# Performance work log

Hardware: AMD Instinct MI355X
Metric: run time of the kernel (lower is better)

## Reference

```python
import jax, jax.numpy as jnp
import numpy as np
import math

B, S, DM, DQ, DK, DV = 4, 4096, 512, 512, 512, 512
MASKED = True


def setup_inputs() -> dict:
    key = jax.random.key(0)
    ks = jax.random.split(key, 9)
    s = 1.0 / math.sqrt(DM)  # ~ torch Linear init scale
    return {
        "q_in": jax.random.normal(ks[0], (B, S, DM), jnp.float32),
        "k_in": jax.random.normal(ks[1], (B, S, DM), jnp.float32),
        "v_in": jax.random.normal(ks[2], (B, S, DM), jnp.float32),
        "Wq": jax.random.uniform(ks[3], (DQ, DM), jnp.float32, -s, s),
        "bq": jax.random.uniform(ks[4], (DQ,), jnp.float32, -s, s),
        "Wk": jax.random.uniform(ks[5], (DK, DM), jnp.float32, -s, s),
        "bk": jax.random.uniform(ks[6], (DK,), jnp.float32, -s, s),
        "Wv": jax.random.uniform(ks[7], (DV, DM), jnp.float32, -s, s),
        "bv": jax.random.uniform(ks[8], (DV,), jnp.float32, -s, s),
    }


def reference(q_in, k_in, v_in, Wq, bq, Wk, bk, Wv, bv):
    # Linear projections (torch Linear: x @ W.T + b)
    q = jnp.einsum("bsm,qm->bsq", q_in, Wq) + bq  # [B,S,DQ]
    k = jnp.einsum("bsm,km->bsk", k_in, Wk) + bk  # [B,S,DK]
    v = jnp.einsum("bsm,vm->bsv", v_in, Wv) + bv  # [B,S,DV]

    scale = 1.0 / math.sqrt(k.shape[-1])
    scores = jnp.einsum("bqd,bkd->bqk", q, k) * scale  # [B,S,S]
    if MASKED:
        # Faithful to torch.tril on the scores: upper triangle set to 0 (NOT -inf)
        tri = jnp.tril(jnp.ones((scores.shape[1], scores.shape[2]), bool))
        scores = jnp.where(tri, scores, jnp.zeros((), scores.dtype))
    attn = jax.nn.softmax(scores, axis=-1)
    return jnp.einsum("bqk,bkv->bqv", attn, v)  # [B,S,DV]
```

## Files before the change

kernel.cpp:

```cpp
#include <hip/hip_runtime.h>

typedef unsigned short u16;
typedef unsigned int   u32;
typedef __bf16  bf16x8 __attribute__((ext_vector_type(8)));
typedef u16     u16x8  __attribute__((ext_vector_type(8)));
typedef float   f32x4  __attribute__((ext_vector_type(4)));

#define S_LEN   4096
#define DMODEL  512
#define NBATCH  4
#define NTILE   32
#define NPAIR   528
#define SCALE   0.044194173824159216f

__device__ __forceinline__ u16 f2bf(float x){
  u32 u = __float_as_uint(x);
  return (u16)((u + 0x7fffu + ((u >> 16) & 1u)) >> 16);
}
__device__ __forceinline__ float bf2f(u16 u){ return __uint_as_float(((u32)u) << 16); }

__device__ __forceinline__ void gload_lds16(const void* g, void* l){
  __builtin_amdgcn_global_load_lds((const __attribute__((address_space(1))) void*)g,
                                   (__attribute__((address_space(3))) void*)l, 16, 0, 0);
}

__global__ __launch_bounds__(256) void cast3_kernel(const float* __restrict__ a,
                                                    const float* __restrict__ b,
                                                    const float* __restrict__ c,
                                                    u16* oa, u16* ob, u16* oc, int n8){
  int z = blockIdx.y;
  const float* in = (z == 0) ? a : (z == 1) ? b : c;
  u16* out = (z == 0) ? oa : (z == 1) ? ob : oc;
  int i = blockIdx.x * 256 + threadIdx.x;
  int stride = gridDim.x * 256;
  for (; i < n8; i += stride){
    const float4* p = (const float4*)in + (size_t)i * 2;
    float4 x = p[0], y = p[1];
    ushort4 o0 = make_ushort4(f2bf(x.x), f2bf(x.y), f2bf(x.z), f2bf(x.w));
    ushort4 o1 = make_ushort4(f2bf(y.x), f2bf(y.y), f2bf(y.z), f2bf(y.w));
    ((ushort4*)out)[(size_t)i*2]   = o0;
    ((ushort4*)out)[(size_t)i*2+1] = o1;
  }
}

__global__ __launch_bounds__(256) void zero_kernel(float* __restrict__ p, int n){
  int i = blockIdx.x * 256 + threadIdx.x;
  if (i < n) p[i] = 0.f;
}

__global__ __launch_bounds__(256) void proj_kernel(
    const u16* __restrict__ qx, const u16* __restrict__ kx, const u16* __restrict__ vx,
    const u16* __restrict__ Wq, const u16* __restrict__ Wk, const u16* __restrict__ Wv,
    const float* __restrict__ bq, const float* __restrict__ bk, const float* __restrict__ bv,
    u16* Qb, u16* Kb, u16* Vb)
{
  __shared__ __align__(16) u16 ldsA[4096], ldsB[4096];
  int z = blockIdx.z;
  const u16* X = (z==0) ? qx : (z==1) ? kx : vx;
  const u16* W = (z==0) ? Wq : (z==1) ? Wk : Wv;
  const float* bias = (z==0) ? bq : (z==1) ? bk : bv;
  u16* Y = (z==0) ? Qb : (z==1) ? Kb : Vb;

  int cn = blockIdx.x, rm = blockIdx.y;
  int t = threadIdx.x, w = t >> 6, l = t & 63, wr = w >> 1, wc = w & 1;
  f32x4 acc[4][4];
  #pragma unroll
  for (int m = 0; m < 4; m++)
    #pragma unroll
    for (int n = 0; n < 4; n++) acc[m][n] = (f32x4){0.f,0.f,0.f,0.f};

  const u16* A = X + (size_t)rm * 128 * DMODEL;
  const u16* B = W + (size_t)cn * 128 * DMODEL;
  int srow = l >> 2, scol = (l & 3) * 8;
  int lo = l & 15, hi = l >> 4;
  for (int s = 0; s < 16; s++){
    #pragma unroll
    for (int cc = 0; cc < 2; ++cc){
      int c = w + cc * 4;
      gload_lds16(A + (size_t)(c*16 + srow)*DMODEL + s*32 + scol, ldsA + c*512);
      gload_lds16(B + (size_t)(c*16 + srow)*DMODEL + s*32 + scol, ldsB + c*512);
    }
    __syncthreads();
    bf16x8 fa[4], fb[4];
    #pragma unroll
    for (int m = 0; m < 4; m++) fa[m] = *(const bf16x8*)(ldsA + (wr*64 + m*16 + lo)*32 + hi*8);
    #pragma unroll
    for (int n = 0; n < 4; n++) fb[n] = *(const bf16x8*)(ldsB + (wc*64 + n*16 + lo)*32 + hi*8);
    #pragma unroll
    for (int m = 0; m < 4; m++)
      #pragma unroll
      for (int n = 0; n < 4; n++)
        acc[m][n] = __builtin_amdgcn_mfma_f32_16x16x32_bf16(fa[m], fb[n], acc[m][n], 0, 0, 0);
    __syncthreads();
  }

  #pragma unroll
  for (int n = 0; n < 4; n++){
    int col = cn*128 + wc*64 + n*16 + lo;
    float bs = bias[col];
    #pragma unroll
    for (int m = 0; m < 4; m++){
      int row0 = rm*128 + wr*64 + m*16 + hi*4;
      #pragma unroll
      for (int j = 0; j < 4; j++)
        Y[(size_t)(row0 + j) * DMODEL + col] = f2bf(acc[m][n][j] + bs);
    }
  }
}

__global__ __launch_bounds__(256) void transpose_kernel(const u16* __restrict__ V,
                                                        u16* __restrict__ Vt)
{
  __shared__ u16 tile[64][66];
  int k0 = blockIdx.x * 64, c0 = blockIdx.y * 64, b = blockIdx.z;
  int t = threadIdx.x;
  #pragma unroll
  for (int i = 0; i < 16; i++){
    int idx = i*256 + t; int r = idx >> 6, c = idx & 63;
    tile[r][c] = V[((size_t)b*S_LEN + k0 + r) * DMODEL + c0 + c];
  }
  __syncthreads();
  #pragma unroll
  for (int i = 0; i < 16; i++){
    int idx = i*256 + t; int r = idx >> 6, c = idx & 63;
    Vt[((size_t)b*DMODEL + c0 + r) * S_LEN + k0 + c] = tile[c][r];
  }
}

__global__ __launch_bounds__(256) void vpart_kernel(const u16* __restrict__ V,
                                                    float* __restrict__ part){
  int t = blockIdx.x, b = blockIdx.y, c = threadIdx.x;
  const u16* base = V + ((size_t)b*S_LEN + t*128) * DMODEL;
  float s0 = 0.f, s1 = 0.f;
  for (int k = 0; k < 128; k++){
    s0 += bf2f(base[(size_t)k*DMODEL + c]);
    s1 += bf2f(base[(size_t)k*DMODEL + 256 + c]);
  }
  part[((size_t)b*NTILE + t)*DMODEL + c]       = s0;
  part[((size_t)b*NTILE + t)*DMODEL + 256 + c] = s1;
}

__global__ void suffix_kernel(const float* __restrict__ part, float* __restrict__ sufx){
  int b = blockIdx.x, c = threadIdx.x;
  float s = 0.f;
  for (int t = NTILE - 1; t >= 0; t--){
    sufx[((size_t)b*NTILE + t)*DMODEL + c] = s;
    s += part[((size_t)b*NTILE + t)*DMODEL + c];
  }
}

__global__ __launch_bounds__(64) void score_kernel(const u16* __restrict__ Q,
                                                   const u16* __restrict__ K,
                                                   u16* __restrict__ P,
                                                   float* __restrict__ Z)
{
  __shared__ __align__(16) u16 ldsA[2][2048], ldsB[2][2048];
  int flat = blockIdx.x;
  int w = (flat & 7) * 1056 + (flat >> 3);
  int b = w / 2112, r = w % 2112;
  int tp = (int)((sqrtf(1.f + 2.f*(float)r) - 1.f) * 0.5f);
  while (2*(tp+1)*(tp+2) <= r) tp++;
  while (2*tp*(tp+1) > r) tp--;
  int rem = r - 2*tp*(tp+1);
  int qi, ki;
  if (rem < 2*tp + 2){ qi = 2*tp; ki = rem; } else { qi = 2*tp + 1; ki = rem - (2*tp + 2); }

  int l = threadIdx.x;
  int lr = l >> 2, lc = (l & 3) * 8;
  int lo = l & 15, hi = l >> 4;

  const u16* A = Q + ((size_t)b*S_LEN + (size_t)qi*64) * DMODEL;
  const u16* B = K + ((size_t)b*S_LEN + (size_t)ki*64) * DMODEL;

  f32x4 acc[4][4];
  #pragma unroll
  for (int m = 0; m < 4; m++)
    #pragma unroll
    for (int n = 0; n < 4; n++) acc[m][n] = (f32x4){0.f,0.f,0.f,0.f};

#define SC_STAGE(tt, buf) { \
    int s32 = (tt)*32; \
    _Pragma("unroll") \
    for (int c = 0; c < 4; c++){ \
      gload_lds16(A + (size_t)(c*16 + lr)*DMODEL + s32 + lc, &ldsA[buf][c*512]); \
      gload_lds16(B + (size_t)(c*16 + lr)*DMODEL + s32 + lc, &ldsB[buf][c*512]); \
    } }

  if (ki <= qi){
    SC_STAGE(0, 0);
    #pragma unroll 2
    for (int tt = 0; tt < 16; ++tt){
      int cur = tt & 1;
      asm volatile("s_waitcnt lgkmcnt(0)" ::: "memory");
      if (tt < 15){
        SC_STAGE(tt + 1, cur ^ 1);
        asm volatile("s_waitcnt vmcnt(8)" ::: "memory");
      } else {
        asm volatile("s_waitcnt vmcnt(0)" ::: "memory");
      }
      __builtin_amdgcn_sched_barrier(0);
      bf16x8 fa[4], fb[4];
      #pragma unroll
      for (int m = 0; m < 4; m++) fa[m] = *(const bf16x8*)(&ldsA[cur][(m*16 + lo)*32 + hi*8]);
      #pragma unroll
      for (int n = 0; n < 4; n++) fb[n] = *(const bf16x8*)(&ldsB[cur][(n*16 + lo)*32 + hi*8]);
      #pragma unroll
      for (int m = 0; m < 4; m++)
        #pragma unroll
        for (int n = 0; n < 4; n++)
          acc[m][n] = __builtin_amdgcn_mfma_f32_16x16x32_bf16(fa[m], fb[n], acc[m][n], 0, 0, 0);
    }
  }
#undef SC_STAGE

  int qt = qi >> 1, kt = ki >> 1;
  u16* Pt = P + ((size_t)b*NPAIR + (size_t)qt*(qt+1)/2 + kt) * 16384
              + (size_t)(qi & 1) * 64 * 128 + (size_t)(ki & 1) * 64;
  #pragma unroll
  for (int m = 0; m < 4; m++){
    #pragma unroll
    for (int j = 0; j < 4; j++){
      int row = m*16 + hi*4 + j;
      int grow = qi*64 + row;
      float rsum = 0.f;
      #pragma unroll
      for (int n = 0; n < 4; n++){
        int col = n*16 + lo;
        int gcol = ki*64 + col;
        float s = (gcol > grow) ? 0.f : acc[m][n][j] * SCALE;
        u16 pb = f2bf(__expf(s));
        Pt[(size_t)row*128 + col] = pb;
        rsum += bf2f(pb);
      }
      rsum += __shfl_xor(rsum, 1);
      rsum += __shfl_xor(rsum, 2);
      rsum += __shfl_xor(rsum, 4);
      rsum += __shfl_xor(rsum, 8);
      if (lo == 0) atomicAdd(&Z[(size_t)b*S_LEN + grow], rsum);
    }
  }
}

__global__ __launch_bounds__(64) void pv_kernel(const u16* __restrict__ P,
                                                const u16* __restrict__ Vt,
                                                const float* __restrict__ sufx,
                                                const float* __restrict__ Z,
                                                float* __restrict__ out)
{
  __shared__ __align__(16) u16 ldsA[2][2048], ldsB[2][2048];
  int flat = (blockIdx.z*64 + blockIdx.y)*8 + blockIdx.x;
  int w = (flat & 7) * 256 + (flat >> 3);
  int b  = w >> 9;
  int qip = (w >> 3) & 63;
  int qi  = (qip & 1) ? (qip >> 1) : 63 - (qip >> 1);
  int ci  = w & 7;
  int qt  = qi >> 1;

  int l = threadIdx.x;
  int lr = l >> 2, lc = (l & 3) * 8;
  int lo = l & 15, hi = l >> 4;

  const u16* Abase = P + ((size_t)b*NPAIR + (size_t)qt*(qt+1)/2) * 16384
                       + (size_t)(qi & 1) * 64 * 128;
  const u16* Bbase = Vt + ((size_t)b*DMODEL + (size_t)ci*64) * S_LEN;

  f32x4 acc[4][4];
  #pragma unroll
  for (int m = 0; m < 4; m++)
    #pragma unroll
    for (int n = 0; n < 4; n++) acc[m][n] = (f32x4){0.f,0.f,0.f,0.f};

  int nstep = (qt + 1) * 4;

#define PV_STAGE(tt, buf) { \
    int kt_ = (tt) >> 2, s_ = ((tt) & 3) * 32; \
    const u16* A_ = Abase + (size_t)kt_*16384 + s_; \
    const u16* B_ = Bbase + kt_*128 + s_; \
    _Pragma("unroll") \
    for (int c = 0; c < 4; c++){ \
      gload_lds16(A_ + (size_t)(c*16 + lr)*128 + lc, &ldsA[buf][c*512]); \
      gload_lds16(B_ + (size_t)(c*16 + lr)*S_LEN + lc, &ldsB[buf][c*512]); \
    } }

  PV_STAGE(0, 0);
  #pragma unroll 2
  for (int tt = 0; tt < nstep; ++tt){
    int cur = tt & 1;
    asm volatile("s_waitcnt lgkmcnt(0)" ::: "memory");
    if (tt + 1 < nstep){
      PV_STAGE(tt + 1, cur ^ 1);
      asm volatile("s_waitcnt vmcnt(8)" ::: "memory");
    } else {
      asm volatile("s_waitcnt vmcnt(0)" ::: "memory");
    }
    __builtin_amdgcn_sched_barrier(0);
    bf16x8 fa[4], fb[4];
    #pragma unroll
    for (int m = 0; m < 4; m++) fa[m] = *(const bf16x8*)(&ldsA[cur][(m*16 + lo)*32 + hi*8]);
    #pragma unroll
    for (int n = 0; n < 4; n++) fb[n] = *(const bf16x8*)(&ldsB[cur][(n*16 + lo)*32 + hi*8]);
    #pragma unroll
    for (int m = 0; m < 4; m++)
      #pragma unroll
      for (int n = 0; n < 4; n++)
        acc[m][n] = __builtin_amdgcn_mfma_f32_16x16x32_bf16(fa[m], fb[n], acc[m][n], 0, 0, 0);
  }
#undef PV_STAGE

  float zadd = (float)(S_LEN - (qt + 1) * 128);
  const float* suf = sufx + ((size_t)b*NTILE + qt)*DMODEL + ci*64;
  const float* Zp  = Z + (size_t)b*S_LEN + (size_t)qi*64;
  float* O = out + ((size_t)b*S_LEN + (size_t)qi*64) * DMODEL + ci*64;
  #pragma unroll
  for (int m = 0; m < 4; m++){
    #pragma unroll
    for (int j = 0; j < 4; j++){
      int row = m*16 + hi*4 + j;
      float rz = 1.f / (Zp[row] + zadd);
      #pragma unroll
      for (int n = 0; n < 4; n++){
        int col = n*16 + lo;
        O[(size_t)row*DMODEL + col] = (acc[m][n][j] + suf[col]) * rz;
      }
    }
  }
}

extern "C" void kernel_launch(void* const* d_in, const int* in_sizes, int n_in,
                              void* d_out, int out_size, void* d_ws, size_t ws_size,
                              hipStream_t stream)
{
  const float* q_in = (const float*)d_in[0];
  const float* k_in = (const float*)d_in[1];
  const float* v_in = (const float*)d_in[2];
  const float* Wq   = (const float*)d_in[3];
  const float* bq   = (const float*)d_in[4];
  const float* Wk   = (const float*)d_in[5];
  const float* bk   = (const float*)d_in[6];
  const float* Wv   = (const float*)d_in[7];
  const float* bv   = (const float*)d_in[8];
  float* out = (float*)d_out;
  char*  ws  = (char*)d_ws;

  const size_t NTOK  = (size_t)NBATCH * S_LEN;
  const size_t TEN_B = NTOK * DMODEL * 2;

  size_t off = 0;
  u16* Wq_b = (u16*)(ws + off); off += DMODEL*DMODEL*2;
  u16* Wk_b = (u16*)(ws + off); off += DMODEL*DMODEL*2;
  u16* Wv_b = (u16*)(ws + off); off += DMODEL*DMODEL*2;
  size_t uoff = off;
  u16* qx = (u16*)(ws + uoff);
  u16* kx = qx + NTOK*DMODEL;
  u16* vx = kx + NTOK*DMODEL;
  u16* Pbuf = (u16*)(ws + uoff);
  size_t usize = (size_t)NBATCH * NPAIR * 16384 * 2;
  off = uoff + usize;
  u16* Qb  = (u16*)(ws + off); off += TEN_B;
  u16* Kb  = (u16*)(ws + off); off += TEN_B;
  u16* Vb  = (u16*)(ws + off); off += TEN_B;
  u16* Vtb = (u16*)(ws + off); off += TEN_B;
  float* part = (float*)(ws + off); off += (size_t)NBATCH*NTILE*DMODEL*4;
  float* sufx = (float*)(ws + off); off += (size_t)NBATCH*NTILE*DMODEL*4;
  float* Zful = (float*)(ws + off); off += (size_t)NBATCH*S_LEN*4;

  int n8_big = (int)(NTOK * DMODEL / 8);
  int n8_w   = DMODEL * DMODEL / 8;
  cast3_kernel<<<dim3(2048, 3), 256, 0, stream>>>(q_in, k_in, v_in, qx, kx, vx, n8_big);
  cast3_kernel<<<dim3(128, 3), 256, 0, stream>>>(Wq, Wk, Wv, Wq_b, Wk_b, Wv_b, n8_w);
  zero_kernel<<<(NBATCH*S_LEN + 255)/256, 256, 0, stream>>>(Zful, NBATCH*S_LEN);

  proj_kernel<<<dim3(DMODEL/128, (unsigned)(NTOK/128), 3), 256, 0, stream>>>(
      qx, kx, vx, Wq_b, Wk_b, Wv_b, bq, bk, bv, Qb, Kb, Vb);

  transpose_kernel<<<dim3(S_LEN/64, DMODEL/64, NBATCH), 256, 0, stream>>>(Vb, Vtb);
  vpart_kernel<<<dim3(NTILE, NBATCH), 256, 0, stream>>>(Vb, part);
  suffix_kernel<<<NBATCH, DMODEL, 0, stream>>>(part, sufx);

  score_kernel<<<8448, 64, 0, stream>>>(Qb, Kb, Pbuf, Zful);
  pv_kernel<<<dim3(8, 64, NBATCH), 64, 0, stream>>>(Pbuf, Vtb, sufx, Zful, out);
}
```

Before: 399.2 us.

## Load MFMA fragments directly from global memory instead of staging through LDS

The projection, score and PV GEMM kernels stop staging tiles through LDS with global_load_lds. Each lane now loads its bf16x8 MFMA operand fragments straight from global memory into registers, using a two-set register double buffer. The projection kernel also shrinks from 256-thread 128x128 tiles to 64-thread 64x64 tiles. This removes LDS traffic, waitcnt handling and barriers, at the cost of strided, less coalesced global loads, lost intra-block reuse, and higher register pressure.

```diff
diff --git a/kernel.cpp b/kernel.cpp
--- a/kernel.cpp
+++ b/kernel.cpp
@@ -19,10 +19,15 @@
 }
 __device__ __forceinline__ float bf2f(u16 u){ return __uint_as_float(((u32)u) << 16); }
 
-__device__ __forceinline__ void gload_lds16(const void* g, void* l){
-  __builtin_amdgcn_global_load_lds((const __attribute__((address_space(1))) void*)g,
-                                   (__attribute__((address_space(3))) void*)l, 16, 0, 0);
-}
+#define MFMA16(aa, bb) { _Pragma("unroll") \
+  for (int m_ = 0; m_ < 4; m_++){ _Pragma("unroll") \
+    for (int n_ = 0; n_ < 4; n_++) \
+      acc[m_][n_] = __builtin_amdgcn_mfma_f32_16x16x32_bf16(aa[m_], bb[n_], acc[m_][n_], 0, 0, 0); } }
+
+#define LOADQK(s_, aa, bb) { _Pragma("unroll") \
+  for (int m_ = 0; m_ < 4; m_++){ \
+    aa[m_] = *(const bf16x8*)(Ap + (size_t)m_*16*DMODEL + (s_)*32); \
+    bb[m_] = *(const bf16x8*)(Bp + (size_t)m_*16*DMODEL + (s_)*32); } }
 
 __global__ __launch_bounds__(256) void cast3_kernel(const float* __restrict__ a,
                                                     const float* __restrict__ b,
@@ -48,13 +53,12 @@
   if (i < n) p[i] = 0.f;
 }
 
-__global__ __launch_bounds__(256) void proj_kernel(
+__global__ __launch_bounds__(64) void proj_kernel(
     const u16* __restrict__ qx, const u16* __restrict__ kx, const u16* __restrict__ vx,
     const u16* __restrict__ Wq, const u16* __restrict__ Wk, const u16* __restrict__ Wv,
     const float* __restrict__ bq, const float* __restrict__ bk, const float* __restrict__ bv,
     u16* Qb, u16* Kb, u16* Vb)
 {
-  __shared__ __align__(16) u16 ldsA[4096], ldsB[4096];
   int z = blockIdx.z;
   const u16* X = (z==0) ? qx : (z==1) ? kx : vx;
   const u16* W = (z==0) ? Wq : (z==1) ? Wk : Wv;
@@ -62,45 +66,33 @@
   u16* Y = (z==0) ? Qb : (z==1) ? Kb : Vb;
 
   int cn = blockIdx.x, rm = blockIdx.y;
-  int t = threadIdx.x, w = t >> 6, l = t & 63, wr = w >> 1, wc = w & 1;
+  int l = threadIdx.x, lo = l & 15, hi = l >> 4;
+
   f32x4 acc[4][4];
   #pragma unroll
   for (int m = 0; m < 4; m++)
     #pragma unroll
     for (int n = 0; n < 4; n++) acc[m][n] = (f32x4){0.f,0.f,0.f,0.f};
 
-  const u16* A = X + (size_t)rm * 128 * DMODEL;
-  const u16* B = W + (size_t)cn * 128 * DMODEL;
-  int srow = l >> 2, scol = (l & 3) * 8;
-  int lo = l & 15, hi = l >> 4;
-  for (int s = 0; s < 16; s++){
-    #pragma unroll
-    for (int cc = 0; cc < 2; ++cc){
-      int c = w + cc * 4;
-      gload_lds16(A + (size_t)(c*16 + srow)*DMODEL + s*32 + scol, ldsA + c*512);
-      gload_lds16(B + (size_t)(c*16 + srow)*DMODEL + s*32 + scol, ldsB + c*512);
-    }
-    __syncthreads();
-    bf16x8 fa[4], fb[4];
-    #pragma unroll
-    for (int m = 0; m < 4; m++) fa[m] = *(const bf16x8*)(ldsA + (wr*64 + m*16 + lo)*32 + hi*8);
-    #pragma unroll
-    for (int n = 0; n < 4; n++) fb[n] = *(const bf16x8*)(ldsB + (wc*64 + n*16 + lo)*32 + hi*8);
-    #pragma unroll
-    for (int m = 0; m < 4; m++)
-      #pragma unroll
-      for (int n = 0; n < 4; n++)
-        acc[m][n] = __builtin_amdgcn_mfma_f32_16x16x32_bf16(fa[m], fb[n], acc[m][n], 0, 0, 0);
-    __syncthreads();
+  const u16* Ap = X + ((size_t)rm*64 + lo) * DMODEL + hi*8;
+  const u16* Bp = W + ((size_t)cn*64 + lo) * DMODEL + hi*8;
+  bf16x8 a0[4], b0[4], a1[4], b1[4];
+  LOADQK(0, a0, b0);
+  #pragma unroll
+  for (int t2 = 0; t2 < 16; t2 += 2){
+    LOADQK(t2+1, a1, b1);
+    MFMA16(a0, b0);
+    if (t2 + 2 < 16) LOADQK(t2+2, a0, b0);
+    MFMA16(a1, b1);
   }
 
   #pragma unroll
   for (int n = 0; n < 4; n++){
-    int col = cn*128 + wc*64 + n*16 + lo;
+    int col = cn*64 + n*16 + lo;
     float bs = bias[col];
     #pragma unroll
     for (int m = 0; m < 4; m++){
-      int row0 = rm*128 + wr*64 + m*16 + hi*4;
+      int row0 = rm*64 + m*16 + hi*4;
       #pragma unroll
       for (int j = 0; j < 4; j++)
         Y[(size_t)(row0 + j) * DMODEL + col] = f2bf(acc[m][n][j] + bs);
@@ -154,7 +146,6 @@
                                                    u16* __restrict__ P,
                                                    float* __restrict__ Z)
 {
-  __shared__ __align__(16) u16 ldsA[2][2048], ldsB[2][2048];
   int flat = blockIdx.x;
   int w = (flat & 7) * 1056 + (flat >> 3);
   int b = w / 2112, r = w % 2112;
@@ -165,12 +156,7 @@
   int qi, ki;
   if (rem < 2*tp + 2){ qi = 2*tp; ki = rem; } else { qi = 2*tp + 1; ki = rem - (2*tp + 2); }
 
-  int l = threadIdx.x;
-  int lr = l >> 2, lc = (l & 3) * 8;
-  int lo = l & 15, hi = l >> 4;
-
-  const u16* A = Q + ((size_t)b*S_LEN + (size_t)qi*64) * DMODEL;
-  const u16* B = K + ((size_t)b*S_LEN + (size_t)ki*64) * DMODEL;
+  int l = threadIdx.x, lo = l & 15, hi = l >> 4;
 
   f32x4 acc[4][4];
   #pragma unroll
@@ -178,40 +164,19 @@
     #pragma unroll
     for (int n = 0; n < 4; n++) acc[m][n] = (f32x4){0.f,0.f,0.f,0.f};
 
-#define SC_STAGE(tt, buf) { \
-    int s32 = (tt)*32; \
-    _Pragma("unroll") \
-    for (int c = 0; c < 4; c++){ \
-      gload_lds16(A + (size_t)(c*16 + lr)*DMODEL + s32 + lc, &ldsA[buf][c*512]); \
-      gload_lds16(B + (size_t)(c*16 + lr)*DMODEL + s32 + lc, &ldsB[buf][c*512]); \
-    } }
-
   if (ki <= qi){
-    SC_STAGE(0, 0);
-    #pragma unroll 2
-    for (int tt = 0; tt < 16; ++tt){
-      int cur = tt & 1;
-      asm volatile("s_waitcnt lgkmcnt(0)" ::: "memory");
-      if (tt < 15){
-        SC_STAGE(tt + 1, cur ^ 1);
-        asm volatile("s_waitcnt vmcnt(8)" ::: "memory");
-      } else {
-        asm volatile("s_waitcnt vmcnt(0)" ::: "memory");
-      }
-      __builtin_amdgcn_sched_barrier(0);
-      bf16x8 fa[4], fb[4];
-      #pragma unroll
-      for (int m = 0; m < 4; m++) fa[m] = *(const bf16x8*)(&ldsA[cur][(m*16 + lo)*32 + hi*8]);
-      #pragma unroll
-      for (int n = 0; n < 4; n++) fb[n] = *(const bf16x8*)(&ldsB[cur][(n*16 + lo)*32 + hi*8]);
-      #pragma unroll
-      for (int m = 0; m < 4; m++)
-        #pragma unroll
-        for (int n = 0; n < 4; n++)
-          acc[m][n] = __builtin_amdgcn_mfma_f32_16x16x32_bf16(fa[m], fb[n], acc[m][n], 0, 0, 0);
+    const u16* Ap = Q + ((size_t)b*S_LEN + (size_t)qi*64 + lo) * DMODEL + hi*8;
+    const u16* Bp = K + ((size_t)b*S_LEN + (size_t)ki*64 + lo) * DMODEL + hi*8;
+    bf16x8 a0[4], b0[4], a1[4], b1[4];
+    LOADQK(0, a0, b0);
+    #pragma unroll
+    for (int t2 = 0; t2 < 16; t2 += 2){
+      LOADQK(t2+1, a1, b1);
+      MFMA16(a0, b0);
+      if (t2 + 2 < 16) LOADQK(t2+2, a0, b0);
+      MFMA16(a1, b1);
     }
   }
-#undef SC_STAGE
 
   int qt = qi >> 1, kt = ki >> 1;
   u16* Pt = P + ((size_t)b*NPAIR + (size_t)qt*(qt+1)/2 + kt) * 16384
@@ -247,7 +212,6 @@
                                                 const float* __restrict__ Z,
                                                 float* __restrict__ out)
 {
-  __shared__ __align__(16) u16 ldsA[2][2048], ldsB[2][2048];
   int flat = (blockIdx.z*64 + blockIdx.y)*8 + blockIdx.x;
   int w = (flat & 7) * 256 + (flat >> 3);
   int b  = w >> 9;
@@ -256,13 +220,11 @@
   int ci  = w & 7;
   int qt  = qi >> 1;
 
-  int l = threadIdx.x;
-  int lr = l >> 2, lc = (l & 3) * 8;
-  int lo = l & 15, hi = l >> 4;
-
-  const u16* Abase = P + ((size_t)b*NPAIR + (size_t)qt*(qt+1)/2) * 16384
-                       + (size_t)(qi & 1) * 64 * 128;
-  const u16* Bbase = Vt + ((size_t)b*DMODEL + (size_t)ci*64) * S_LEN;
+  int l = threadIdx.x, lo = l & 15, hi = l >> 4;
+
+  const u16* Ap = P + ((size_t)b*NPAIR + (size_t)qt*(qt+1)/2) * 16384
+                    + (size_t)(qi & 1) * 64 * 128 + (size_t)lo * 128 + hi*8;
+  const u16* Bp = Vt + ((size_t)b*DMODEL + (size_t)ci*64 + lo) * S_LEN + hi*8;
 
   f32x4 acc[4][4];
   #pragma unroll
@@ -272,40 +234,22 @@
 
   int nstep = (qt + 1) * 4;
 
-#define PV_STAGE(tt, buf) { \
-    int kt_ = (tt) >> 2, s_ = ((tt) & 3) * 32; \
-    const u16* A_ = Abase + (size_t)kt_*16384 + s_; \
-    const u16* B_ = Bbase + kt_*128 + s_; \
+#define LOADPV(tt_, aa, bb) { int kt_ = (tt_) >> 2, s4_ = ((tt_) & 3) * 32; \
     _Pragma("unroll") \
-    for (int c = 0; c < 4; c++){ \
-      gload_lds16(A_ + (size_t)(c*16 + lr)*128 + lc, &ldsA[buf][c*512]); \
-      gload_lds16(B_ + (size_t)(c*16 + lr)*S_LEN + lc, &ldsB[buf][c*512]); \
-    } }
-
-  PV_STAGE(0, 0);
-  #pragma unroll 2
-  for (int tt = 0; tt < nstep; ++tt){
-    int cur = tt & 1;
-    asm volatile("s_waitcnt lgkmcnt(0)" ::: "memory");
-    if (tt + 1 < nstep){
-      PV_STAGE(tt + 1, cur ^ 1);
-      asm volatile("s_waitcnt vmcnt(8)" ::: "memory");
-    } else {
-      asm volatile("s_waitcnt vmcnt(0)" ::: "memory");
-    }
-    __builtin_amdgcn_sched_barrier(0);
-    bf16x8 fa[4], fb[4];
-    #pragma unroll
-    for (int m = 0; m < 4; m++) fa[m] = *(const bf16x8*)(&ldsA[cur][(m*16 + lo)*32 + hi*8]);
-    #pragma unroll
-    for (int n = 0; n < 4; n++) fb[n] = *(const bf16x8*)(&ldsB[cur][(n*16 + lo)*32 + hi*8]);
-    #pragma unroll
-    for (int m = 0; m < 4; m++)
-      #pragma unroll
-      for (int n = 0; n < 4; n++)
-        acc[m][n] = __builtin_amdgcn_mfma_f32_16x16x32_bf16(fa[m], fb[n], acc[m][n], 0, 0, 0);
-  }
-#undef PV_STAGE
+    for (int m_ = 0; m_ < 4; m_++){ \
+      aa[m_] = *(const bf16x8*)(Ap + (size_t)kt_*16384 + (size_t)m_*2048 + s4_); \
+      bb[m_] = *(const bf16x8*)(Bp + (size_t)(tt_)*32 + (size_t)m_*16*S_LEN); } }
+
+  bf16x8 a0[4], b0[4], a1[4], b1[4];
+  LOADPV(0, a0, b0);
+  #pragma unroll 1
+  for (int t2 = 0; t2 < nstep; t2 += 2){
+    LOADPV(t2+1, a1, b1);
+    MFMA16(a0, b0);
+    if (t2 + 2 < nstep) LOADPV(t2+2, a0, b0);
+    MFMA16(a1, b1);
+  }
+#undef LOADPV
 
   float zadd = (float)(S_LEN - (qt + 1) * 128);
   const float* suf = sufx + ((size_t)b*NTILE + qt)*DMODEL + ci*64;
@@ -370,7 +314,7 @@
   cast3_kernel<<<dim3(128, 3), 256, 0, stream>>>(Wq, Wk, Wv, Wq_b, Wk_b, Wv_b, n8_w);
   zero_kernel<<<(NBATCH*S_LEN + 255)/256, 256, 0, stream>>>(Zful, NBATCH*S_LEN);
 
-  proj_kernel<<<dim3(DMODEL/128, (unsigned)(NTOK/128), 3), 256, 0, stream>>>(
+  proj_kernel<<<dim3(DMODEL/64, (unsigned)(NTOK/64), 3), 64, 0, stream>>>(
       qx, kx, vx, Wq_b, Wk_b, Wv_b, bq, bk, bv, Qb, Kb, Vb);
 
   transpose_kernel<<<dim3(S_LEN/64, DMODEL/64, NBATCH), 256, 0, stream>>>(Vb, Vtb);
```

Measured after the change: 607.1 us. +52.1%, slower.
